# Performance work log

Hardware: AMD Instinct MI355X
Metric: run time of the kernel (lower is better)

Reference implementation:

```python
import jax, jax.numpy as jnp
import numpy as np

K = 7          # kernel_size
PAD = 3        # padding (same-size output)
GROUPS = 8


def _unfold(z, H, W):
    # z: [B, C, H+2p, W+2p] -> patches [B, C, H, W, K*K], flat index = kh*K + kw
    # matches torch .unfold(2,K,1).unfold(3,K,1).view(..., -1)
    return jnp.stack(
        [z[:, :, a:a + H, b:b + W] for a in range(K) for b in range(K)],
        axis=-1,
    )


def setup_inputs() -> dict:
    key = jax.random.key(0)
    ks = jax.random.split(key, 7)
    B, C, H, W = 4, 64, 64, 64
    Cout = 64
    fan_scale = (2.0 / Cout) ** 0.5  # kaiming fan_out, 1x1 conv
    return {
        "x": jax.random.normal(ks[0], (B, C, H, W), jnp.float32),
        "y": jax.random.normal(ks[1], (B, C, H, W), jnp.float32),
        "Wq": jax.random.normal(ks[2], (Cout, C), jnp.float32) * fan_scale,
        "Wk": jax.random.normal(ks[3], (Cout, C), jnp.float32) * fan_scale,
        "Wv": jax.random.normal(ks[4], (Cout, C), jnp.float32) * fan_scale,
        "rel_h": jax.random.normal(ks[5], (Cout // 2, K), jnp.float32),
        "rel_w": jax.random.normal(ks[6], (Cout // 2, K), jnp.float32),
    }


def reference(x, y, Wq, Wk, Wv, rel_h, rel_w):
    B, C, H, W = x.shape
    Cout = Wq.shape[0]
    half = Cout // 2

    # 1x1 convs (no bias) commute with zero padding, so project first.
    q = jnp.einsum('oc,bchw->bohw', Wq, x)          # [B, Cout, H, W]
    k_full = jnp.einsum('oc,bchw->bohw', Wk, x)
    v_full = jnp.einsum('oc,bchw->bohw', Wv, y)

    pad4 = ((0, 0), (0, 0), (PAD, PAD), (PAD, PAD))
    k_pat = _unfold(jnp.pad(k_full, pad4), H, W)    # [B, Cout, H, W, K*K]
    v_pat = _unfold(jnp.pad(v_full, pad4), H, W)

    # relative-position bias: rel_h over kh (top half of channels), rel_w over kw
    bias_h = jnp.broadcast_to(rel_h[:, :, None], (half, K, K))   # [Cout/2, kh, kw]
    bias_w = jnp.broadcast_to(rel_w[:, None, :], (half, K, K))
    bias = jnp.concatenate([bias_h, bias_w], axis=0).reshape(Cout, K * K)
    k_pat = k_pat + bias[None, :, None, None, :]

    cg = Cout // GROUPS
    k_pat = k_pat.reshape(B, GROUPS, cg, H, W, K * K)
    v_pat = v_pat.reshape(B, GROUPS, cg, H, W, K * K)
    q = q.reshape(B, GROUPS, cg, H, W, 1)

    attn = jax.nn.softmax(q * k_pat, axis=-1)       # per-channel softmax over window
    out = jnp.sum(attn * v_pat, axis=-1)            # [B, G, cg, H, W]
    return out.reshape(B, Cout, H, W)
```

## Files before the change

kernel.cpp:

```cpp
#include <hip/hip_runtime.h>

#define HW 4096

typedef float f4 __attribute__((ext_vector_type(4)));
typedef float f2 __attribute__((ext_vector_type(2)));

__global__ __launch_bounds__(256) void proj_kernel(
    const float* __restrict__ x, const float* __restrict__ y,
    const float* __restrict__ Wq, const float* __restrict__ Wk,
    const float* __restrict__ Wv,
    float* __restrict__ qkv)
{
    const int sp = blockIdx.x >> 5;
    const int m  = sp >> 3;
    const int r0 = (sp & 7) * 8;
    const int pi = (blockIdx.x & 31) * 256 + threadIdx.x;
    const int px = pi * 2;
    const int b  = px >> 12;
    const int pp = px & 4095;

    const float* W   = (m == 0) ? Wq : (m == 1) ? Wk : Wv;
    const float* src = (m == 2) ? y : x;
    const float* sb  = src + (size_t)b * 64 * HW + pp;

    f2 acc[8];
#pragma unroll
    for (int j = 0; j < 8; ++j) acc[j] = (f2){0.f, 0.f};

#pragma unroll
    for (int cb = 0; cb < 8; ++cb) {
        f2 xv[8];
#pragma unroll
        for (int c2 = 0; c2 < 8; ++c2)
            xv[c2] = *(const f2*)&sb[(cb * 8 + c2) * HW];
#pragma unroll
        for (int j = 0; j < 8; ++j) {
            const float* wr = W + (r0 + j) * 64 + cb * 8;
#pragma unroll
            for (int c2 = 0; c2 < 8; ++c2) {
                acc[j][0] = fmaf(wr[c2], xv[c2][0], acc[j][0]);
                acc[j][1] = fmaf(wr[c2], xv[c2][1], acc[j][1]);
            }
        }
    }

    float* dstm = qkv + ((size_t)m << 20) + (size_t)b * 64 * HW + pp;
#pragma unroll
    for (int j = 0; j < 8; ++j)
        *(f2*)&dstm[(size_t)(r0 + j) * HW] = acc[j];
}

__global__ __launch_bounds__(256) void attn_kernel(
    const float* __restrict__ qg, const float* __restrict__ kg,
    const float* __restrict__ vg,
    const float* __restrict__ rel_h, const float* __restrict__ rel_w,
    float* __restrict__ out)
{
    __shared__ float kT[22 * 72];
    __shared__ float vT[22 * 72];

    const int blk = blockIdx.x;
    const int bc  = blk >> 2;
    const int h0  = (blk & 3) << 4;
    const int c   = bc & 63;
    const int t   = threadIdx.x;

    const float* kimg = kg + (size_t)bc * HW;
    const float* vimg = vg + (size_t)bc * HW;
    const f4 z4 = {0.f, 0.f, 0.f, 0.f};

    if (t < 88) {
        const int row = t >> 2, side = (t >> 1) & 1, arr = t & 1;
        float* dst = arr ? vT : kT;
        *(f4*)&dst[row * 72 + side * 68] = z4;
    }
#pragma unroll
    for (int j = 0; j < 2; ++j) {
        const int idx = j * 256 + t;
        if (idx < 352) {
            const int row = idx >> 4, ch = idx & 15;
            const int hy = h0 - 3 + row;
            const bool rv = ((unsigned)hy < 64u);
            const f4 kv = rv ? *(const f4*)&kimg[hy * 64 + ch * 4] : z4;
            const f4 vv = rv ? *(const f4*)&vimg[hy * 64 + ch * 4] : z4;
            *(f4*)&kT[row * 72 + ch * 4 + 4] = kv;
            *(f4*)&vT[row * 72 + ch * 4 + 4] = vv;
        }
    }
    __syncthreads();

    const int r  = t >> 4;
    const int w0 = (t & 15) << 2;
    const int h  = h0 + r;

    const float LOG2E = 1.4426950408889634f;
    const f4 qv = *(const f4*)&qg[(size_t)bc * HW + h * 64 + w0];
    float qe[4];
#pragma unroll
    for (int p = 0; p < 4; ++p) qe[p] = qv[p] * LOG2E;

    float qb[7][4];
    if (c < 32) {
#pragma unroll
        for (int a = 0; a < 7; ++a) {
            const float bb = rel_h[c * 7 + a];
#pragma unroll
            for (int p = 0; p < 4; ++p) qb[a][p] = qe[p] * bb;
        }
    } else {
#pragma unroll
        for (int j = 0; j < 7; ++j) {
            const float bb = rel_w[(c - 32) * 7 + j];
#pragma unroll
            for (int p = 0; p < 4; ++p) qb[j][p] = qe[p] * bb;
        }
    }

    float l[4] = {0.f, 0.f, 0.f, 0.f};
    float o[4] = {0.f, 0.f, 0.f, 0.f};

    if (c < 32) {
#pragma unroll
        for (int a = 0; a < 7; ++a) {
            const int ro = (r + a) * 72 + w0;
            const f4 k0 = *(const f4*)&kT[ro];
            const f4 k1 = *(const f4*)&kT[ro + 4];
            const f4 k2 = *(const f4*)&kT[ro + 8];
            const f4 v0 = *(const f4*)&vT[ro];
            const f4 v1 = *(const f4*)&vT[ro + 4];
            const f4 v2 = *(const f4*)&vT[ro + 8];
            const float kw[12] = {k0[0], k0[1], k0[2], k0[3], k1[0], k1[1], k1[2], k1[3],
                                  k2[0], k2[1], k2[2], k2[3]};
            const float vw[12] = {v0[0], v0[1], v0[2], v0[3], v1[0], v1[1], v1[2], v1[3],
                                  v2[0], v2[1], v2[2], v2[3]};
#pragma unroll
            for (int b2 = 0; b2 < 7; ++b2)
#pragma unroll
                for (int p = 0; p < 4; ++p) {
                    const float s = fmaf(qe[p], kw[p + b2 + 1], qb[a][p]);
                    const float e = __builtin_amdgcn_exp2f(s);
                    l[p] += e;
                    o[p] = fmaf(e, vw[p + b2 + 1], o[p]);
                }
        }
    } else {
#pragma unroll
        for (int a = 0; a < 7; ++a) {
            const int ro = (r + a) * 72 + w0;
            const f4 k0 = *(const f4*)&kT[ro];
            const f4 k1 = *(const f4*)&kT[ro + 4];
            const f4 k2 = *(const f4*)&kT[ro + 8];
            const f4 v0 = *(const f4*)&vT[ro];
            const f4 v1 = *(const f4*)&vT[ro + 4];
            const f4 v2 = *(const f4*)&vT[ro + 8];
            const float kw[12] = {k0[0], k0[1], k0[2], k0[3], k1[0], k1[1], k1[2], k1[3],
                                  k2[0], k2[1], k2[2], k2[3]};
            const float vw[12] = {v0[0], v0[1], v0[2], v0[3], v1[0], v1[1], v1[2], v1[3],
                                  v2[0], v2[1], v2[2], v2[3]};
#pragma unroll
            for (int b2 = 0; b2 < 7; ++b2)
#pragma unroll
                for (int p = 0; p < 4; ++p) {
                    const float s = fmaf(qe[p], kw[p + b2 + 1], qb[b2][p]);
                    const float e = __builtin_amdgcn_exp2f(s);
                    l[p] += e;
                    o[p] = fmaf(e, vw[p + b2 + 1], o[p]);
                }
        }
    }

    f4 res;
#pragma unroll
    for (int p = 0; p < 4; ++p)
        res[p] = o[p] * __builtin_amdgcn_rcpf(l[p]);
    *(f4*)&out[(size_t)bc * HW + h * 64 + w0] = res;
}

extern "C" void kernel_launch(void* const* d_in, const int* in_sizes, int n_in,
                              void* d_out, int out_size, void* d_ws, size_t ws_size,
                              hipStream_t stream) {
    const float* x   = (const float*)d_in[0];
    const float* y   = (const float*)d_in[1];
    const float* Wq  = (const float*)d_in[2];
    const float* Wk  = (const float*)d_in[3];
    const float* Wv  = (const float*)d_in[4];
    const float* rlh = (const float*)d_in[5];
    const float* rlw = (const float*)d_in[6];
    float* out = (float*)d_out;

    float* qkv = (float*)d_ws;
    float* q = qkv;
    float* k = qkv + (1 << 20);
    float* v = qkv + (2 << 20);

    proj_kernel<<<768, 256, 0, stream>>>(x, y, Wq, Wk, Wv, qkv);
    attn_kernel<<<1024, 256, 0, stream>>>(q, k, v, rlh, rlw, out);
}
```

Baseline: 94.65 us.

## Restructure projection kernel to share x loads across Q and K outputs

The projection kernel is reorganised so each block covers 32 pixels and all output channels. Q and K are computed together from one read of x, with each thread producing 4 channels for 4 pixels. Previously every 8-row slice re-read the input channels, so input traffic drops and loads widen to f4. The V part uses 512 separate blocks, and the grid grows from 768 to 1024. The cost is fewer pixels per block with redundant L1/L2 traffic, and Q/K threads carry more register pressure.

```diff
diff --git a/kernel.cpp b/kernel.cpp
--- a/kernel.cpp
+++ b/kernel.cpp
@@ -3,7 +3,6 @@
 #define HW 4096
 
 typedef float f4 __attribute__((ext_vector_type(4)));
-typedef float f2 __attribute__((ext_vector_type(2)));
 
 __global__ __launch_bounds__(256) void proj_kernel(
     const float* __restrict__ x, const float* __restrict__ y,
@@ -11,43 +10,85 @@
     const float* __restrict__ Wv,
     float* __restrict__ qkv)
 {
-    const int sp = blockIdx.x >> 5;
-    const int m  = sp >> 3;
-    const int r0 = (sp & 7) * 8;
-    const int pi = (blockIdx.x & 31) * 256 + threadIdx.x;
-    const int px = pi * 2;
-    const int b  = px >> 12;
-    const int pp = px & 4095;
-
-    const float* W   = (m == 0) ? Wq : (m == 1) ? Wk : Wv;
-    const float* src = (m == 2) ? y : x;
-    const float* sb  = src + (size_t)b * 64 * HW + pp;
-
-    f2 acc[8];
-#pragma unroll
-    for (int j = 0; j < 8; ++j) acc[j] = (f2){0.f, 0.f};
-
-#pragma unroll
-    for (int cb = 0; cb < 8; ++cb) {
-        f2 xv[8];
-#pragma unroll
-        for (int c2 = 0; c2 < 8; ++c2)
-            xv[c2] = *(const f2*)&sb[(cb * 8 + c2) * HW];
-#pragma unroll
-        for (int j = 0; j < 8; ++j) {
-            const float* wr = W + (r0 + j) * 64 + cb * 8;
-#pragma unroll
-            for (int c2 = 0; c2 < 8; ++c2) {
-                acc[j][0] = fmaf(wr[c2], xv[c2][0], acc[j][0]);
-                acc[j][1] = fmaf(wr[c2], xv[c2][1], acc[j][1]);
+    const int t   = threadIdx.x;
+    const int blk = blockIdx.x;
+    const int pxq = t & 7;
+    const int cg  = t >> 3;
+
+    if (blk < 512) {
+        const int p0 = blk * 32;
+        const int b  = p0 >> 12;
+        const int pp = (p0 & 4095) + pxq * 4;
+        const int r0 = cg * 4;
+        const float* xb = x + (size_t)b * 64 * HW + pp;
+        const float* Wb = (r0 < 64) ? (Wq + r0 * 64) : (Wk + (r0 - 64) * 64);
+
+        f4 acc[4];
+#pragma unroll
+        for (int j = 0; j < 4; ++j) acc[j] = (f4){0.f, 0.f, 0.f, 0.f};
+
+#pragma unroll
+        for (int cb = 0; cb < 8; ++cb) {
+            f4 xv[8];
+#pragma unroll
+            for (int c2 = 0; c2 < 8; ++c2)
+                xv[c2] = *(const f4*)&xb[(cb * 8 + c2) * HW];
+#pragma unroll
+            for (int j = 0; j < 4; ++j) {
+                const float* wr = Wb + j * 64 + cb * 8;
+                const f4 w0 = *(const f4*)&wr[0];
+                const f4 w1 = *(const f4*)&wr[4];
+#pragma unroll
+                for (int c2 = 0; c2 < 4; ++c2) {
+                    acc[j] += xv[c2] * w0[c2];
+                    acc[j] += xv[c2 + 4] * w1[c2];
+                }
             }
         }
-    }
-
-    float* dstm = qkv + ((size_t)m << 20) + (size_t)b * 64 * HW + pp;
-#pragma unroll
-    for (int j = 0; j < 8; ++j)
-        *(f2*)&dstm[(size_t)(r0 + j) * HW] = acc[j];
+
+        const int m = (r0 >= 64);
+        float* dst = qkv + ((size_t)m << 20)
+                         + ((size_t)b * 64 + (r0 & 63)) * HW + pp;
+#pragma unroll
+        for (int j = 0; j < 4; ++j)
+            *(f4*)&dst[(size_t)j * HW] = acc[j];
+    } else {
+        const int p0 = (blk - 512) * 32;
+        const int b  = p0 >> 12;
+        const int pp = (p0 & 4095) + pxq * 4;
+        const int r0 = cg * 2;
+        const float* yb = y + (size_t)b * 64 * HW + pp;
+        const float* Wb = Wv + r0 * 64;
+
+        f4 acc[2];
+#pragma unroll
+        for (int j = 0; j < 2; ++j) acc[j] = (f4){0.f, 0.f, 0.f, 0.f};
+
+#pragma unroll
+        for (int cb = 0; cb < 8; ++cb) {
+            f4 yv[8];
+#pragma unroll
+            for (int c2 = 0; c2 < 8; ++c2)
+                yv[c2] = *(const f4*)&yb[(cb * 8 + c2) * HW];
+#pragma unroll
+            for (int j = 0; j < 2; ++j) {
+                const float* wr = Wb + j * 64 + cb * 8;
+                const f4 w0 = *(const f4*)&wr[0];
+                const f4 w1 = *(const f4*)&wr[4];
+#pragma unroll
+                for (int c2 = 0; c2 < 4; ++c2) {
+                    acc[j] += yv[c2] * w0[c2];
+                    acc[j] += yv[c2 + 4] * w1[c2];
+                }
+            }
+        }
+
+        float* dst = qkv + ((size_t)2 << 20)
+                         + ((size_t)b * 64 + r0) * HW + pp;
+#pragma unroll
+        for (int j = 0; j < 2; ++j)
+            *(f4*)&dst[(size_t)j * HW] = acc[j];
+    }
 }
 
 __global__ __launch_bounds__(256) void attn_kernel(
@@ -193,6 +234,6 @@
     float* k = qkv + (1 << 20);
     float* v = qkv + (2 << 20);
 
-    proj_kernel<<<768, 256, 0, stream>>>(x, y, Wq, Wk, Wv, qkv);
+    proj_kernel<<<1024, 256, 0, stream>>>(x, y, Wq, Wk, Wv, qkv);
     attn_kernel<<<1024, 256, 0, stream>>>(q, k, v, rlh, rlw, out);
 }
```

New measurement: 98.91 us. 1.04x slower.
